# Kernel optimization log

Hardware: AMD Instinct MI355X
Metric: run time of the kernel (lower is better)

## Reference

```python
import jax, jax.numpy as jnp
import numpy as np

IMG, P, CIN, D, K, L, H, FF, B = 512, 32, 3, 256, 8192, 6, 8, 1024, 32
GRID = IMG // P  # 16
DH = D // H
EPS = 1e-5


def _ln(x, w, b):
    m = x.mean(-1, keepdims=True)
    v = ((x - m) ** 2).mean(-1, keepdims=True)
    return (x - m) / jnp.sqrt(v + EPS) * w + b


def _mha(x, wqkv, bqkv, wo, bo):
    # x: (S, Bt, D) -- axis 0 is the attention axis (torch batch_first=False quirk)
    S, Bt, _ = x.shape
    qkv = x @ wqkv.T + bqkv
    q, k, v = jnp.split(qkv, 3, axis=-1)
    q = q.reshape(S, Bt, H, DH)
    k = k.reshape(S, Bt, H, DH)
    v = v.reshape(S, Bt, H, DH)
    scores = jnp.einsum('sbhd,tbhd->bhst', q, k) / jnp.sqrt(jnp.float32(DH))
    attn = jax.nn.softmax(scores, axis=-1)
    o = jnp.einsum('bhst,tbhd->sbhd', attn, v).reshape(S, Bt, D)
    return o @ wo.T + bo


def _conv_t(x, w, b, stride=2, pad=1):
    # w uses torch ConvTranspose2d layout (Cin, Cout, kH, kW)
    kH = w.shape[2]
    wf = jnp.flip(w, (2, 3)).transpose(1, 0, 2, 3)  # -> (Cout, Cin, kH, kW)
    y = jax.lax.conv_general_dilated(
        x, wf, window_strides=(1, 1),
        padding=[(kH - 1 - pad, kH - 1 - pad)] * 2,
        lhs_dilation=(stride, stride),
        dimension_numbers=('NCHW', 'OIHW', 'NCHW'))
    return y + b[None, :, None, None]


def _forward(x, patch_w, patch_b, qkv_w, qkv_b, out_w, out_b, ln1_w, ln1_b,
             ln2_w, ln2_b, ff1_w, ff1_b, ff2_w, ff2_b, lnf_w, lnf_b, codebook,
             dec_w0, dec_b0, dec_w1, dec_b1, dec_w2, dec_b2, dec_w3, dec_b3):
    # patch embedding: conv stride=patch -> (B, D, G, G) -> (B, N, D)
    h = jax.lax.conv_general_dilated(
        x, patch_w, (P, P), 'VALID',
        dimension_numbers=('NCHW', 'OIHW', 'NCHW')) + patch_b[None, :, None, None]
    h = h.reshape(h.shape[0], D, -1).transpose(0, 2, 1)  # (B, N, D)
    # torch TransformerEncoderLayer default batch_first=False: attention runs
    # over axis 0 (image batch); faithfully replicated here. Post-norm, eval
    # mode (dropout=identity), exact gelu.
    for i in range(L):
        a = _mha(h, qkv_w[i], qkv_b[i], out_w[i], out_b[i])
        h = _ln(h + a, ln1_w[i], ln1_b[i])
        f = jax.nn.gelu(h @ ff1_w[i].T + ff1_b[i], approximate=False) @ ff2_w[i].T + ff2_b[i]
        h = _ln(h + f, ln2_w[i], ln2_b[i])
    h = _ln(h, lnf_w, lnf_b)
    # vector quantization: squared-distance argmin over codebook
    flat = h.reshape(-1, D)  # (B*N, D)
    d = ((flat ** 2).sum(-1, keepdims=True)
         - 2.0 * flat @ codebook.T
         + (codebook ** 2).sum(-1))  # (B*N, K)
    idx = jnp.argmin(d, axis=1)
    q = codebook[idx].reshape(h.shape)
    e_loss = jnp.mean((jax.lax.stop_gradient(q) - h) ** 2)
    q_loss = jnp.mean((q - jax.lax.stop_gradient(h)) ** 2)
    vq_loss = q_loss + 0.25 * e_loss
    q = h + jax.lax.stop_gradient(q - h)  # straight-through
    q = q.transpose(0, 2, 1).reshape(x.shape[0], D, GRID, GRID)
    y = jax.nn.relu(_conv_t(q, dec_w0, dec_b0))
    y = jax.nn.relu(_conv_t(y, dec_w1, dec_b1))
    y = jax.nn.relu(_conv_t(y, dec_w2, dec_b2))
    x_hat = jax.nn.sigmoid(_conv_t(y, dec_w3, dec_b3))
    return x_hat, vq_loss


def setup_inputs() -> dict:
    key = jax.random.key(0)
    ks = iter(jax.random.split(key, 64))
    nrm = lambda shape, s=0.02: jax.random.normal(next(ks), shape, jnp.float32) * s
    f32 = jnp.float32
    return {
        'x': jax.random.normal(next(ks), (B, CIN, IMG, IMG), f32),
        'patch_w': nrm((D, CIN, P, P)),
        'patch_b': jnp.zeros((D,), f32),
        'qkv_w': nrm((L, 3 * D, D)),
        'qkv_b': jnp.zeros((L, 3 * D), f32),
        'out_w': nrm((L, D, D)),
        'out_b': jnp.zeros((L, D), f32),
        'ln1_w': jnp.ones((L, D), f32),
        'ln1_b': jnp.zeros((L, D), f32),
        'ln2_w': jnp.ones((L, D), f32),
        'ln2_b': jnp.zeros((L, D), f32),
        'ff1_w': nrm((L, FF, D)),
        'ff1_b': jnp.zeros((L, FF), f32),
        'ff2_w': nrm((L, D, FF)),
        'ff2_b': jnp.zeros((L, D), f32),
        'lnf_w': jnp.ones((D,), f32),
        'lnf_b': jnp.zeros((D,), f32),
        'codebook': jax.random.uniform(next(ks), (K, D), f32, -1.0 / K, 1.0 / K),
        'dec_w0': nrm((D, 256, 4, 4)),
        'dec_b0': jnp.zeros((256,), f32),
        'dec_w1': nrm((256, 128, 4, 4)),
        'dec_b1': jnp.zeros((128,), f32),
        'dec_w2': nrm((128, 64, 4, 4)),
        'dec_b2': jnp.zeros((64,), f32),
        'dec_w3': nrm((64, CIN, 4, 4)),
        'dec_b3': jnp.zeros((CIN,), f32),
    }


def reference(x, patch_w, patch_b, qkv_w, qkv_b, out_w, out_b, ln1_w, ln1_b,
              ln2_w, ln2_b, ff1_w, ff1_b, ff2_w, ff2_b, lnf_w, lnf_b, codebook,
              dec_w0, dec_b0, dec_w1, dec_b1, dec_w2, dec_b2, dec_w3, dec_b3):
    return _forward(x, patch_w, patch_b, qkv_w, qkv_b, out_w, out_b, ln1_w,
                    ln1_b, ln2_w, ln2_b, ff1_w, ff1_b, ff2_w, ff2_b, lnf_w,
                    lnf_b, codebook, dec_w0, dec_b0, dec_w1, dec_b1, dec_w2,
                    dec_b2, dec_w3, dec_b3)
```

## Files before the change

kernel.cpp:

```cpp
#include <hip/hip_runtime.h>
#include <hip/hip_bf16.h>
#include <math.h>

typedef __hip_bfloat16 bf16;
typedef unsigned int u32;
typedef unsigned long long u64;
using short8 = __attribute__((ext_vector_type(8))) short;
using f32x4  = __attribute__((ext_vector_type(4))) float;

__device__ __forceinline__ float b2f(bf16 v){ return __bfloat162float(v); }
__device__ __forceinline__ bf16  f2b(float v){ return __float2bfloat16(v); }
__device__ __forceinline__ float plo(u32 u){ return __uint_as_float(u << 16); }
__device__ __forceinline__ float phi(u32 u){ return __uint_as_float(u & 0xffff0000u); }

__device__ __forceinline__ void gld16(const void* g, void* l)
{
  __builtin_amdgcn_global_load_lds(
      (const __attribute__((address_space(1))) u32*)g,
      (__attribute__((address_space(3))) u32*)l, 16, 0, 0);
}

__global__ void k_detect(const u32* probe, int* flag)
{
  if (threadIdx.x == 0 && blockIdx.x == 0)
    *flag = (*probe == 0x3F800000u) ? 0 : 1;
}

struct PPack { const void* s[25]; u32 off[26]; };
__global__ __launch_bounds__(256) void k_convall(PPack pp, bf16* P, const int* flag)
{
  const u32 i = blockIdx.x * 256 + threadIdx.x;
  if (i >= pp.off[25]) return;
  int lo = 0, hi = 25;
  while (hi - lo > 1) { const int mid = (lo + hi) >> 1; if (i >= pp.off[mid]) lo = mid; else hi = mid; }
  const u32 j = i - pp.off[lo];
  P[i] = *flag ? ((const bf16*)pp.s[lo])[j] : f2b(((const float*)pp.s[lo])[j]);
}

__global__ __launch_bounds__(256) void k_zero(u32* p, int n)
{
  const int i = blockIdx.x * 256 + threadIdx.x;
  if (i < n) p[i] = 0;
}

__global__ __launch_bounds__(128) void k_im2col(const void* x, bf16* A, const int* flag)
{
  const int m = blockIdx.y;
  const int k8 = blockIdx.x * 128 + threadIdx.x;
  const int k = k8 * 8;
  const int b = m >> 8, n = m & 255;
  const int gy = n >> 4, gx = n & 15;
  const int c = k >> 10, r = (k >> 5) & 31, pp = k & 31;
  const size_t src = (((size_t)(b * 3 + c) * 512) + gy * 32 + r) * 512 + gx * 32 + pp;
  bf16 ov[8];
  if (*flag) {
    const bf16* xp = (const bf16*)x + src;
    #pragma unroll
    for (int i = 0; i < 8; ++i) ov[i] = xp[i];
  } else {
    const float4 v0 = *reinterpret_cast<const float4*>((const float*)x + src);
    const float4 v1 = *reinterpret_cast<const float4*>((const float*)x + src + 4);
    ov[0]=f2b(v0.x); ov[1]=f2b(v0.y); ov[2]=f2b(v0.z); ov[3]=f2b(v0.w);
    ov[4]=f2b(v1.x); ov[5]=f2b(v1.y); ov[6]=f2b(v1.z); ov[7]=f2b(v1.w);
  }
  *reinterpret_cast<uint4*>(A + (size_t)m * 3072 + k) = *reinterpret_cast<const uint4*>(ov);
}

template<int EPI, int FM>
__global__ __launch_bounds__(256, 2) void gemm_t(
    const bf16* __restrict__ A, const bf16* __restrict__ Bw,
    const bf16* __restrict__ bias, const bf16* res, bf16* C,
    const float* __restrict__ cnorm, u64* __restrict__ ku,
    int M, int N, int K)
{
  constexpr int BM = FM * 32;
  __shared__ alignas(16) bf16 As[2][BM * 64];
  __shared__ alignas(16) bf16 Bs[2][128 * 64];
  const int tid = threadIdx.x;
  const int bn = blockIdx.x * 128, bm = blockIdx.y * BM;
  const int l = tid & 63, w = tid >> 6;
  const int wm = w >> 1, wn = w & 1;
  const int lg = l >> 4, lr = l & 15;
  const int sr8 = l >> 3;
  const int sch = (l & 7) ^ sr8;
  f32x4 acc[FM][4];
  #pragma unroll
  for (int fm = 0; fm < FM; ++fm)
    #pragma unroll
    for (int fn = 0; fn < 4; ++fn) acc[fm][fn] = (f32x4){0.f, 0.f, 0.f, 0.f};

  auto stage = [&](int bb, int k0) {
    char* ab = (char*)As[bb];
    char* bp = (char*)Bs[bb];
    #pragma unroll
    for (int it = 0; it < FM; ++it) {
      const int r = w * 8 + it * 32 + sr8;
      gld16(A + (size_t)(bm + r) * K + k0 + sch * 8, ab + w * 1024 + it * 4096);
    }
    #pragma unroll
    for (int it = 0; it < 4; ++it) {
      const int r = w * 8 + it * 32 + sr8;
      gld16(Bw + (size_t)(bn + r) * K + k0 + sch * 8, bp + w * 1024 + it * 4096);
    }
  };

  const int nt = K >> 6;
  stage(0, 0);
  __syncthreads();
  for (int t = 0; t < nt; ++t) {
    const int cur = t & 1;
    if (t + 1 < nt) stage(cur ^ 1, (t + 1) << 6);
    const char* ab = (const char*)As[cur];
    const char* bb = (const char*)Bs[cur];
    #pragma unroll
    for (int ks = 0; ks < 2; ++ks) {
      short8 af[FM], bfr[4];
      #pragma unroll
      for (int fm = 0; fm < FM; ++fm) {
        const int r = wm * (FM * 16) + fm * 16 + lr;
        af[fm] = *reinterpret_cast<const short8*>(ab + r * 128 + (((lg + ks * 4) ^ (r & 7)) * 16));
      }
      #pragma unroll
      for (int fn = 0; fn < 4; ++fn) {
        const int r = wn * 64 + fn * 16 + lr;
        bfr[fn] = *reinterpret_cast<const short8*>(bb + r * 128 + (((lg + ks * 4) ^ (r & 7)) * 16));
      }
      #pragma unroll
      for (int fm = 0; fm < FM; ++fm)
        #pragma unroll
        for (int fn = 0; fn < 4; ++fn)
          acc[fm][fn] = __builtin_amdgcn_mfma_f32_16x16x32_bf16(af[fm], bfr[fn], acc[fm][fn], 0, 0, 0);
    }
    __syncthreads();
  }

  if (EPI == 3) {
    __shared__ u64 skey[128][2];
    float cn4[4];
    #pragma unroll
    for (int fn = 0; fn < 4; ++fn) cn4[fn] = cnorm[bn + wn * 64 + fn * 16 + lr];
    #pragma unroll
    for (int fm = 0; fm < FM; ++fm) {
      #pragma unroll
      for (int r = 0; r < 4; ++r) {
        u64 best = ~0ull;
        #pragma unroll
        for (int fn = 0; fn < 4; ++fn) {
          const int col = bn + wn * 64 + fn * 16 + lr;
          const float d = cn4[fn] - 2.0f * acc[fm][fn][r];
          u32 u = __float_as_uint(d);
          u = (u & 0x80000000u) ? ~u : (u | 0x80000000u);
          const u64 key = ((u64)u << 32) | (u32)col;
          best = key < best ? key : best;
        }
        #pragma unroll
        for (int mk = 1; mk < 16; mk <<= 1) {
          const u64 o = __shfl_xor(best, mk, 64);
          best = o < best ? o : best;
        }
        if (lr == 0) skey[wm * 64 + fm * 16 + lg * 4 + r][wn] = best;
      }
    }
    __syncthreads();
    if (tid < 128) {
      const u64 a = skey[tid][0], b = skey[tid][1];
      ku[(size_t)blockIdx.x * M + bm + tid] = a < b ? a : b;
    }
  } else {
    #pragma unroll
    for (int fm = 0; fm < FM; ++fm) {
      const int m0 = bm + wm * (FM * 16) + fm * 16 + lg * 4;
      #pragma unroll
      for (int fn = 0; fn < 4; ++fn) {
        const int n = bn + wn * 64 + fn * 16 + lr;
        const float bs = b2f(bias[n]);
        #pragma unroll
        for (int r = 0; r < 4; ++r) {
          float v = acc[fm][fn][r] + bs;
          if (EPI == 1) v = 0.5f * v * (1.0f + erff(v * 0.70710678118654752f));
          if (EPI == 2) v += b2f(res[(size_t)(m0 + r) * N + n]);
          C[(size_t)(m0 + r) * N + n] = f2b(v);
        }
      }
    }
  }
}

__global__ __launch_bounds__(256) void k_vqmerge(
    const u64* __restrict__ ku, int* __restrict__ idx, int M, int NB)
{
  const int r = blockIdx.x * 256 + threadIdx.x;
  if (r >= M) return;
  u64 best = ku[r];
  for (int nb = 1; nb < NB; ++nb) {
    const u64 k = ku[(size_t)nb * M + r];
    best = k < best ? k : best;
  }
  idx[r] = (int)(best & 0xFFFFFFFFull);
}

__global__ __launch_bounds__(256) void k_cnorm(const bf16* __restrict__ cb, float* __restrict__ cn)
{
  const int j = blockIdx.x * 256 + threadIdx.x;
  const u32* p = (const u32*)(cb + (size_t)j * 256);
  float s = 0.f;
  for (int k = 0; k < 128; ++k) {
    const u32 v = p[k];
    const float a = plo(v), b = phi(v);
    s += a * a + b * b;
  }
  cn[j] = s;
}

__global__ __launch_bounds__(256) void k_ln(
    bf16* h, const bf16* w, const bf16* b)
{
  __shared__ float red[256];
  __shared__ float stat[2];
  const int row = blockIdx.x, d = threadIdx.x;
  const size_t base = (size_t)row * 256;
  const float x = b2f(h[base + d]);
  red[d] = x;
  __syncthreads();
  for (int off = 128; off > 0; off >>= 1) {
    if (d < off) red[d] += red[d + off];
    __syncthreads();
  }
  if (d == 0) stat[0] = red[0] * (1.0f / 256.0f);
  __syncthreads();
  const float m = stat[0];
  red[d] = (x - m) * (x - m);
  __syncthreads();
  for (int off = 128; off > 0; off >>= 1) {
    if (d < off) red[d] += red[d + off];
    __syncthreads();
  }
  if (d == 0) stat[1] = 1.0f / sqrtf(red[0] * (1.0f / 256.0f) + 1e-5f);
  __syncthreads();
  h[base + d] = f2b((x - m) * stat[1] * b2f(w[d]) + b2f(b[d]));
}

__global__ __launch_bounds__(256) void k_attn(
    const bf16* qkv, bf16* o)
{
  __shared__ float qs[32][33], ks[32][33], vs[32][33], ps[32][33];
  __shared__ float rs[32];
  const int bt = blockIdx.x, hd = blockIdx.y;
  const int tid = threadIdx.x;
  for (int e = 0; e < 4; ++e) {
    const int elem = tid + 256 * e;
    const int s = elem >> 5, c = elem & 31;
    const bf16* p = qkv + (size_t)(s * 256 + bt) * 768 + hd * 32 + c;
    qs[s][c] = b2f(p[0]);
    ks[s][c] = b2f(p[256]);
    vs[s][c] = b2f(p[512]);
  }
  __syncthreads();
  const int s = tid >> 3, j = tid & 7;
  float sc[4];
  #pragma unroll
  for (int e = 0; e < 4; ++e) {
    const int t = j + 8 * e;
    float v = 0.f;
    #pragma unroll
    for (int dd = 0; dd < 32; ++dd) v += qs[s][dd] * ks[t][dd];
    sc[e] = v * 0.17677669529663687f;
  }
  float mx = fmaxf(fmaxf(sc[0], sc[1]), fmaxf(sc[2], sc[3]));
  #pragma unroll
  for (int mk = 1; mk < 8; mk <<= 1) mx = fmaxf(mx, __shfl_xor(mx, mk, 64));
  float sm = 0.f; float ex[4];
  #pragma unroll
  for (int e = 0; e < 4; ++e) { ex[e] = expf(sc[e] - mx); sm += ex[e]; }
  #pragma unroll
  for (int mk = 1; mk < 8; mk <<= 1) sm += __shfl_xor(sm, mk, 64);
  #pragma unroll
  for (int e = 0; e < 4; ++e) ps[s][j + 8 * e] = ex[e];
  if (j == 0) rs[s] = 1.0f / sm;
  __syncthreads();
  #pragma unroll
  for (int e = 0; e < 4; ++e) {
    const int dd = j + 8 * e;
    float acc = 0.f;
    #pragma unroll
    for (int t = 0; t < 32; ++t) acc += ps[s][t] * vs[t][dd];
    o[(size_t)(s * 256 + bt) * 256 + hd * 32 + dd] = f2b(acc * rs[s]);
  }
}

__global__ __launch_bounds__(256) void k_gather(
    const bf16* h, const bf16* cb, const int* idx, bf16* a0, float* lsum)
{
  __shared__ float red[256];
  const int row = blockIdx.x, d = threadIdx.x;
  const int code = idx[row] & 8191;
  const float q = b2f(cb[(size_t)code * 256 + d]);
  const float x = b2f(h[(size_t)row * 256 + d]);
  red[d] = (q - x) * (q - x);
  __syncthreads();
  for (int off = 128; off > 0; off >>= 1) {
    if (d < off) red[d] += red[d + off];
    __syncthreads();
  }
  if (d == 0) lsum[row] = red[0];
  const int b = row >> 8, n = row & 255;
  const int y = n >> 4, xc = n & 15;
  a0[(((size_t)b * 18 + y + 1) * 18 + (xc + 1)) * 256 + d] = f2b(q);
}

__global__ __launch_bounds__(256) void k_loss(const float* lsum, float* out)
{
  __shared__ float red[256];
  const int tid = threadIdx.x;
  float v = 0.f;
  for (int i = 0; i < 32; ++i) v += lsum[tid + 256 * i];
  red[tid] = v;
  __syncthreads();
  for (int off = 128; off > 0; off >>= 1) {
    if (tid < off) red[tid] += red[tid + off];
    __syncthreads();
  }
  if (tid == 0)
    out[0] = red[0] * (1.25f / 2097152.0f);
}

__global__ __launch_bounds__(256) void k_wtrans(
    const bf16* __restrict__ w, bf16* __restrict__ wt,
    int Cin, int lCin, int CoutR, int CoutP)
{
  const int K = Cin << 2;
  const int total = 4 * CoutP * K;
  const int i = blockIdx.x * 256 + threadIdx.x;
  if (i >= total) return;
  const int p = i / (CoutP * K);
  const int rem = i - p * (CoutP * K);
  const int co = rem / K;
  const int k = rem - co * K;
  const int tap = k >> lCin, ci = k - (tap << lCin);
  const int py = p >> 1, px = p & 1, ty = tap >> 1, tx = tap & 1;
  bf16 v = f2b(0.f);
  if (co < CoutR)
    v = w[(((size_t)ci * CoutR + co) * 4 + py + 2 * ty) * 4 + px + 2 * tx];
  wt[i] = v;
}

__global__ __launch_bounds__(256, 2) void convt64(
    const bf16* __restrict__ in, const bf16* __restrict__ Wt,
    const bf16* __restrict__ bias, bf16* __restrict__ outp,
    int H, int lH, int Cin, int lCin, int Cout)
{
  __shared__ alignas(16) bf16 As[2][128 * 64];
  __shared__ alignas(16) bf16 Bs[2][64 * 64];
  const int tid = threadIdx.x;
  const int pz = blockIdx.z;
  const int py = pz >> 1, px = pz & 1;
  const int K = Cin << 2;
  const int bn = blockIdx.x * 64, bm = blockIdx.y * 128;
  const bf16* Bw = Wt + (size_t)pz * Cout * K;
  const int l = tid & 63, w = tid >> 6;
  const int wm = w >> 1, wn = w & 1;
  const int lg = l >> 4, lr = l & 15;
  const int sr8 = l >> 3;
  const int sch = (l & 7) ^ sr8;
  const int Hp = H + 2;
  f32x4 acc[4][2];
  #pragma unroll
  for (int fm = 0; fm < 4; ++fm)
    #pragma unroll
    for (int fn = 0; fn < 2; ++fn) acc[fm][fn] = (f32x4){0.f, 0.f, 0.f, 0.f};

  size_t pixbase[4];
  #pragma unroll
  for (int it = 0; it < 4; ++it) {
    const int m = bm + w * 8 + it * 32 + sr8;
    const int b = m >> (2 * lH);
    const int rem = m & ((1 << (2 * lH)) - 1);
    const int jj = rem >> lH, ii = rem & (H - 1);
    pixbase[it] = ((size_t)(b * Hp + jj) * Hp + ii);
  }

  auto stage = [&](int bb, int k0) {
    char* ab = (char*)As[bb];
    char* bp = (char*)Bs[bb];
    const int tap = k0 >> lCin;
    const int ty = tap >> 1, tx = tap & 1;
    const int sy = (1 - py) + (1 - ty);
    const int sx = (1 - px) + (1 - tx);
    const int ci0 = (k0 - (tap << lCin)) + sch * 8;
    #pragma unroll
    for (int it = 0; it < 4; ++it)
      gld16(in + (pixbase[it] + (size_t)sy * Hp + sx) * Cin + ci0,
            ab + w * 1024 + it * 4096);
    #pragma unroll
    for (int it = 0; it < 2; ++it) {
      const int r = w * 8 + it * 32 + sr8;
      gld16(Bw + (size_t)(bn + r) * K + k0 + sch * 8, bp + w * 1024 + it * 4096);
    }
  };

  const int nt = K >> 6;
  stage(0, 0);
  __syncthreads();
  for (int t = 0; t < nt; ++t) {
    const int cur = t & 1;
    if (t + 1 < nt) stage(cur ^ 1, (t + 1) << 6);
    const char* ab = (const char*)As[cur];
    const char* bb = (const char*)Bs[cur];
    #pragma unroll
    for (int ks = 0; ks < 2; ++ks) {
      short8 af[4], bfr[2];
      #pragma unroll
      for (int fm = 0; fm < 4; ++fm) {
        const int r = wm * 64 + fm * 16 + lr;
        af[fm] = *reinterpret_cast<const short8*>(ab + r * 128 + (((lg + ks * 4) ^ (r & 7)) * 16));
      }
      #pragma unroll
      for (int fn = 0; fn < 2; ++fn) {
        const int r = wn * 32 + fn * 16 + lr;
        bfr[fn] = *reinterpret_cast<const short8*>(bb + r * 128 + (((lg + ks * 4) ^ (r & 7)) * 16));
      }
      #pragma unroll
      for (int fm = 0; fm < 4; ++fm)
        #pragma unroll
        for (int fn = 0; fn < 2; ++fn)
          acc[fm][fn] = __builtin_amdgcn_mfma_f32_16x16x32_bf16(af[fm], bfr[fn], acc[fm][fn], 0, 0, 0);
    }
    __syncthreads();
  }

  const int Ho = 2 * H, Hop = Ho + 2;
  #pragma unroll
  for (int fm = 0; fm < 4; ++fm) {
    const int m0 = bm + wm * 64 + fm * 16 + lg * 4;
    #pragma unroll
    for (int fn = 0; fn < 2; ++fn) {
      const int n = bn + wn * 32 + fn * 16 + lr;
      #pragma unroll
      for (int r = 0; r < 4; ++r) {
        const int m = m0 + r;
        const int b = m >> (2 * lH);
        const int rem = m & ((1 << (2 * lH)) - 1);
        const int jj = rem >> lH, ii = rem & (H - 1);
        const int oy = 2 * jj + (1 - py), ox = 2 * ii + (1 - px);
        const float v = fmaxf(acc[fm][fn][r] + b2f(bias[n]), 0.f);
        outp[((size_t)(b * Hop + oy + 1) * Hop + ox + 1) * Cout + n] = f2b(v);
      }
    }
  }
}

__global__ __launch_bounds__(256) void k_dec3(
    const bf16* __restrict__ a3, const bf16* __restrict__ wt3,
    const bf16* __restrict__ bias, float* __restrict__ xhat, int chunkBase)
{
  __shared__ float wl[4][3][256];
  const int tid = threadIdx.x;
  for (int i = tid; i < 3072; i += 256) {
    const int pz = i / 768;
    const int rem = i - pz * 768;
    const int co = rem >> 8, k = rem & 255;
    wl[pz][co][k] = b2f(wt3[(pz * 3 + co) * 256 + k]);
  }
  __syncthreads();
  const int b = blockIdx.y;
  const int t = blockIdx.x;
  const int oy = (t >> 4) * 16 + (tid >> 4);
  const int ox = (t & 15) * 16 + (tid & 15);
  const int py = (oy + 1) & 1, px = (ox + 1) & 1;
  const int jj = (oy - 1 + py) >> 1, ii = (ox - 1 + px) >> 1;
  const int pz = py * 2 + px;
  float a0 = 0.f, a1 = 0.f, a2 = 0.f;
  #pragma unroll
  for (int ty = 0; ty < 2; ++ty) {
    #pragma unroll
    for (int tx = 0; tx < 2; ++tx) {
      const int sy = (1 - py) + (1 - ty), sx = (1 - px) + (1 - tx);
      const int tap = ty * 2 + tx;
      const u32* ip = (const u32*)(a3 + ((size_t)(b * 130 + jj + sy) * 130 + ii + sx) * 64);
      const float* w0 = &wl[pz][0][tap * 64];
      const float* w1 = &wl[pz][1][tap * 64];
      const float* w2 = &wl[pz][2][tap * 64];
      #pragma unroll
      for (int kk = 0; kk < 32; ++kk) {
        const u32 v = ip[kk];
        const float e0 = plo(v), e1 = phi(v);
        a0 += e0 * w0[2 * kk] + e1 * w0[2 * kk + 1];
        a1 += e0 * w1[2 * kk] + e1 * w1[2 * kk + 1];
        a2 += e0 * w2[2 * kk] + e1 * w2[2 * kk + 1];
      }
    }
  }
  const int n = chunkBase + b;
  const size_t ob = (size_t)n * 3 * 65536 + oy * 256 + ox;
  xhat[ob]           = 1.0f / (1.0f + expf(-(a0 + b2f(bias[0]))));
  xhat[ob + 65536]   = 1.0f / (1.0f + expf(-(a1 + b2f(bias[1]))));
  xhat[ob + 131072]  = 1.0f / (1.0f + expf(-(a2 + b2f(bias[2]))));
}

extern "C" void kernel_launch(void* const* d_in, const int* in_sizes, int n_in,
                              void* d_out, int out_size, void* d_ws, size_t ws_size,
                              hipStream_t stream)
{
  float* xhat = (float*)d_out;
  float* lossout = xhat + (out_size - 1);

  const size_t NEED = 130195456;
  if (ws_size < NEED) return;

  char* ws = (char*)d_ws;
  int*   flag  = (int*)  (ws + 0);
  float* lsum  = (float*)(ws + 1024);
  int*   idx   = (int*)  (ws + 65536);
  u64*   ku    = (u64*)  (ws + 131072);
  bf16*  P     = (bf16*) (ws + 8519680);
  bf16*  WT    = (bf16*) (ws + 27262976);
  float* cnorm = (float*)(ws + 30900224);
  bf16*  hbuf  = (bf16*) (ws + 31457280);
  bf16*  A_im  = (bf16*) (ws + 35651584);
  bf16*  qkvb  = (bf16*) (ws + 35651584);
  bf16*  obuf  = (bf16*) (ws + 48234496);
  bf16*  ffb   = (bf16*) (ws + 52428800);
  bf16*  a0    = (bf16*) (ws + 35651584);
  bf16*  a1    = (bf16*) (ws + 40960000);
  bf16*  a2    = (bf16*) (ws + 59899904);
  bf16*  a3    = (bf16*) (ws + 95584256);

  k_detect<<<1, 64, 0, stream>>>((const u32*)d_in[7], flag);

  size_t poff[26]; poff[1] = 0;
  for (int i = 2; i <= 25; ++i) poff[i] = poff[i - 1] + (size_t)in_sizes[i - 1];
  const size_t ptotal = poff[25] + (size_t)in_sizes[25];
  PPack pp;
  for (int i = 0; i < 25; ++i) { pp.s[i] = d_in[i + 1]; pp.off[i] = (u32)poff[i + 1]; }
  pp.off[25] = (u32)ptotal;
  k_convall<<<(int)((ptotal + 255) / 256), 256, 0, stream>>>(pp, P, flag);

  const bf16 *patch_w = P + poff[1],  *patch_b = P + poff[2];
  const bf16 *qkv_w   = P + poff[3],  *qkv_b   = P + poff[4];
  const bf16 *out_w   = P + poff[5],  *out_b   = P + poff[6];
  const bf16 *ln1_w   = P + poff[7],  *ln1_b   = P + poff[8];
  const bf16 *ln2_w   = P + poff[9],  *ln2_b   = P + poff[10];
  const bf16 *ff1_w   = P + poff[11], *ff1_b   = P + poff[12];
  const bf16 *ff2_w   = P + poff[13], *ff2_b   = P + poff[14];
  const bf16 *lnf_w   = P + poff[15], *lnf_b   = P + poff[16];
  const bf16 *codebook= P + poff[17];
  const bf16 *dec_w0  = P + poff[18], *dec_b0  = P + poff[19];
  const bf16 *dec_w1  = P + poff[20], *dec_b1  = P + poff[21];
  const bf16 *dec_w2  = P + poff[22], *dec_b2  = P + poff[23];
  const bf16 *dec_w3  = P + poff[24], *dec_b3  = P + poff[25];

  bf16* wt0 = WT;
  bf16* wt1 = wt0 + 1048576;
  bf16* wt2 = wt1 + 524288;
  bf16* wt3 = wt2 + 131072;
  k_wtrans<<<(1048576 + 255) / 256, 256, 0, stream>>>(dec_w0, wt0, 256, 8, 256, 256);
  k_wtrans<<<(524288 + 255) / 256, 256, 0, stream>>>(dec_w1, wt1, 256, 8, 128, 128);
  k_wtrans<<<(131072 + 255) / 256, 256, 0, stream>>>(dec_w2, wt2, 128, 7, 64, 64);
  k_wtrans<<<(3072 + 255) / 256, 256, 0, stream>>>(dec_w3, wt3, 64, 6, 3, 3);
  k_cnorm<<<32, 256, 0, stream>>>(codebook, cnorm);

  k_im2col<<<dim3(3, 8192), 128, 0, stream>>>(d_in[0], A_im, flag);
  gemm_t<0, 1><<<dim3(2, 256), 256, 0, stream>>>(
      A_im, patch_w, patch_b, nullptr, hbuf, nullptr, nullptr, 8192, 256, 3072);

  for (int l = 0; l < 6; ++l) {
    gemm_t<0, 2><<<dim3(6, 128), 256, 0, stream>>>(
        hbuf, qkv_w + (size_t)l * 768 * 256, qkv_b + l * 768, nullptr, qkvb,
        nullptr, nullptr, 8192, 768, 256);
    k_attn<<<dim3(256, 8), 256, 0, stream>>>(qkvb, obuf);
    gemm_t<2, 1><<<dim3(2, 256), 256, 0, stream>>>(
        obuf, out_w + (size_t)l * 256 * 256, out_b + l * 256, hbuf, hbuf,
        nullptr, nullptr, 8192, 256, 256);
    k_ln<<<8192, 256, 0, stream>>>(hbuf, ln1_w + l * 256, ln1_b + l * 256);
    gemm_t<1, 2><<<dim3(8, 128), 256, 0, stream>>>(
        hbuf, ff1_w + (size_t)l * 1024 * 256, ff1_b + l * 1024, nullptr, ffb,
        nullptr, nullptr, 8192, 1024, 256);
    gemm_t<2, 1><<<dim3(2, 256), 256, 0, stream>>>(
        ffb, ff2_w + (size_t)l * 256 * 1024, ff2_b + l * 256, hbuf, hbuf,
        nullptr, nullptr, 8192, 256, 1024);
    k_ln<<<8192, 256, 0, stream>>>(hbuf, ln2_w + l * 256, ln2_b + l * 256);
  }
  k_ln<<<8192, 256, 0, stream>>>(hbuf, lnf_w, lnf_b);

  gemm_t<3, 4><<<dim3(64, 64), 256, 0, stream>>>(
      hbuf, codebook, nullptr, nullptr, nullptr, cnorm, ku, 8192, 8192, 256);
  k_vqmerge<<<32, 256, 0, stream>>>(ku, idx, 8192, 64);

  k_zero<<<(1327104 + 255) / 256, 256, 0, stream>>>((u32*)a0, 1327104);
  k_gather<<<8192, 256, 0, stream>>>(hbuf, codebook, idx, a0, lsum);
  k_loss<<<1, 256, 0, stream>>>(lsum, lossout);

  k_zero<<<(4734976 + 255) / 256, 256, 0, stream>>>((u32*)a1, 4734976);
  k_zero<<<(8921088 + 255) / 256, 256, 0, stream>>>((u32*)a2, 8921088);
  k_zero<<<(8652800 + 255) / 256, 256, 0, stream>>>((u32*)a3, 8652800);

  convt64<<<dim3(4, 64, 4), 256, 0, stream>>>(a0, wt0, dec_b0, a1, 16, 4, 256, 8, 256);
  convt64<<<dim3(2, 256, 4), 256, 0, stream>>>(a1, wt1, dec_b1, a2, 32, 5, 256, 8, 128);
  for (int c = 0; c < 2; ++c) {
    const bf16* a2c = a2 + (size_t)c * 16 * 66 * 66 * 128;
    convt64<<<dim3(1, 512, 4), 256, 0, stream>>>(a2c, wt2, dec_b2, a3, 64, 6, 128, 7, 64);
    k_dec3<<<dim3(256, 16), 256, 0, stream>>>(a3, wt3, dec_b3, xhat, c * 16);
  }
}
```

Before: 1.156 ms.

## Split-K narrow GEMMs into fp32 partials and fuse reduction with bias, residual, LayerNorm

The N=256 GEMMs (patch embed, attention out-proj, FF2) now use split-K over blockIdx.z and write fp32 partials. A new row kernel sums the partials, adds bias and residual, and applies LayerNorm in the same pass. This replaces the separate residual epilogue and k_ln launches and adds more blocks for the long-K GEMMs. The GEMM also gains a single-buffered mode for the short-K cases, which halves LDS so more blocks can be resident, at the cost of losing load/compute overlap. The trade-off is extra fp32 partial traffic to and from global memory in exchange for more parallelism and fewer bf16 round trips.

```diff
diff --git a/kernel.cpp b/kernel.cpp
--- a/kernel.cpp
+++ b/kernel.cpp
@@ -66,18 +66,20 @@
   *reinterpret_cast<uint4*>(A + (size_t)m * 3072 + k) = *reinterpret_cast<const uint4*>(ov);
 }
 
-template<int EPI, int FM>
+template<int EPI, int FM, bool DB>
 __global__ __launch_bounds__(256, 2) void gemm_t(
     const bf16* __restrict__ A, const bf16* __restrict__ Bw,
-    const bf16* __restrict__ bias, const bf16* res, bf16* C,
+    const bf16* __restrict__ bias, bf16* C, float* __restrict__ Cf,
     const float* __restrict__ cnorm, u64* __restrict__ ku,
-    int M, int N, int K)
+    int M, int N, int K, int Kc)
 {
   constexpr int BM = FM * 32;
-  __shared__ alignas(16) bf16 As[2][BM * 64];
-  __shared__ alignas(16) bf16 Bs[2][128 * 64];
+  __shared__ alignas(16) bf16 As[DB ? 2 : 1][BM * 64];
+  __shared__ alignas(16) bf16 Bs[DB ? 2 : 1][128 * 64];
   const int tid = threadIdx.x;
   const int bn = blockIdx.x * 128, bm = blockIdx.y * BM;
+  const int z = blockIdx.z;
+  const int kb = z * Kc;
   const int l = tid & 63, w = tid >> 6;
   const int wm = w >> 1, wn = w & 1;
   const int lg = l >> 4, lr = l & 15;
@@ -103,15 +105,9 @@
       gld16(Bw + (size_t)(bn + r) * K + k0 + sch * 8, bp + w * 1024 + it * 4096);
     }
   };
-
-  const int nt = K >> 6;
-  stage(0, 0);
-  __syncthreads();
-  for (int t = 0; t < nt; ++t) {
-    const int cur = t & 1;
-    if (t + 1 < nt) stage(cur ^ 1, (t + 1) << 6);
-    const char* ab = (const char*)As[cur];
-    const char* bb = (const char*)Bs[cur];
+  auto compute = [&](int bb) {
+    const char* ab = (const char*)As[bb];
+    const char* bp = (const char*)Bs[bb];
     #pragma unroll
     for (int ks = 0; ks < 2; ++ks) {
       short8 af[FM], bfr[4];
@@ -123,7 +119,7 @@
       #pragma unroll
       for (int fn = 0; fn < 4; ++fn) {
         const int r = wn * 64 + fn * 16 + lr;
-        bfr[fn] = *reinterpret_cast<const short8*>(bb + r * 128 + (((lg + ks * 4) ^ (r & 7)) * 16));
+        bfr[fn] = *reinterpret_cast<const short8*>(bp + r * 128 + (((lg + ks * 4) ^ (r & 7)) * 16));
       }
       #pragma unroll
       for (int fm = 0; fm < FM; ++fm)
@@ -131,7 +127,25 @@
         for (int fn = 0; fn < 4; ++fn)
           acc[fm][fn] = __builtin_amdgcn_mfma_f32_16x16x32_bf16(af[fm], bfr[fn], acc[fm][fn], 0, 0, 0);
     }
-    __syncthreads();
+  };
+
+  const int nt = Kc >> 6;
+  if (DB) {
+    stage(0, kb);
+    __syncthreads();
+    for (int t = 0; t < nt; ++t) {
+      const int cur = t & 1;
+      if (t + 1 < nt) stage(cur ^ 1, kb + ((t + 1) << 6));
+      compute(cur);
+      __syncthreads();
+    }
+  } else {
+    for (int t = 0; t < nt; ++t) {
+      if (t) __syncthreads();
+      stage(0, kb + (t << 6));
+      __syncthreads();
+      compute(0);
+    }
   }
 
   if (EPI == 3) {
@@ -166,6 +180,18 @@
       const u64 a = skey[tid][0], b = skey[tid][1];
       ku[(size_t)blockIdx.x * M + bm + tid] = a < b ? a : b;
     }
+  } else if (EPI == 4) {
+    #pragma unroll
+    for (int fm = 0; fm < FM; ++fm) {
+      const int m0 = bm + wm * (FM * 16) + fm * 16 + lg * 4;
+      #pragma unroll
+      for (int fn = 0; fn < 4; ++fn) {
+        const int n = bn + wn * 64 + fn * 16 + lr;
+        #pragma unroll
+        for (int r = 0; r < 4; ++r)
+          Cf[((size_t)z * M + m0 + r) * N + n] = acc[fm][fn][r];
+      }
+    }
   } else {
     #pragma unroll
     for (int fm = 0; fm < FM; ++fm) {
@@ -178,12 +204,45 @@
         for (int r = 0; r < 4; ++r) {
           float v = acc[fm][fn][r] + bs;
           if (EPI == 1) v = 0.5f * v * (1.0f + erff(v * 0.70710678118654752f));
-          if (EPI == 2) v += b2f(res[(size_t)(m0 + r) * N + n]);
           C[(size_t)(m0 + r) * N + n] = f2b(v);
         }
       }
     }
   }
+}
+
+template<bool DOLN>
+__global__ __launch_bounds__(256) void k_lnred(
+    const float* __restrict__ Pf, const bf16* __restrict__ bias,
+    const bf16* res, const bf16* __restrict__ lw, const bf16* __restrict__ lb,
+    bf16* h, int kc)
+{
+  __shared__ float red[256];
+  __shared__ float stat[2];
+  const int row = blockIdx.x, d = threadIdx.x;
+  float s = 0.f;
+  for (int z = 0; z < kc; ++z) s += Pf[((size_t)z * 8192 + row) * 256 + d];
+  s += b2f(bias[d]);
+  if (res) s += b2f(res[(size_t)row * 256 + d]);
+  if (!DOLN) { h[(size_t)row * 256 + d] = f2b(s); return; }
+  red[d] = s;
+  __syncthreads();
+  for (int off = 128; off > 0; off >>= 1) {
+    if (d < off) red[d] += red[d + off];
+    __syncthreads();
+  }
+  if (d == 0) stat[0] = red[0] * (1.0f / 256.0f);
+  __syncthreads();
+  const float m = stat[0];
+  red[d] = (s - m) * (s - m);
+  __syncthreads();
+  for (int off = 128; off > 0; off >>= 1) {
+    if (d < off) red[d] += red[d + off];
+    __syncthreads();
+  }
+  if (d == 0) stat[1] = 1.0f / sqrtf(red[0] * (1.0f / 256.0f) + 1e-5f);
+  __syncthreads();
+  h[(size_t)row * 256 + d] = f2b((s - m) * stat[1] * b2f(lw[d]) + b2f(lb[d]));
 }
 
 __global__ __launch_bounds__(256) void k_vqmerge(
@@ -520,6 +579,7 @@
   bf16*  qkvb  = (bf16*) (ws + 35651584);
   bf16*  obuf  = (bf16*) (ws + 48234496);
   bf16*  ffb   = (bf16*) (ws + 52428800);
+  float* Pf    = (float*)(ws + 85983232);
   bf16*  a0    = (bf16*) (ws + 35651584);
   bf16*  a1    = (bf16*) (ws + 40960000);
   bf16*  a2    = (bf16*) (ws + 59899904);
@@ -560,30 +620,34 @@
   k_cnorm<<<32, 256, 0, stream>>>(codebook, cnorm);
 
   k_im2col<<<dim3(3, 8192), 128, 0, stream>>>(d_in[0], A_im, flag);
-  gemm_t<0, 1><<<dim3(2, 256), 256, 0, stream>>>(
-      A_im, patch_w, patch_b, nullptr, hbuf, nullptr, nullptr, 8192, 256, 3072);
+  gemm_t<4, 2, true><<<dim3(2, 128, 4), 256, 0, stream>>>(
+      A_im, patch_w, nullptr, nullptr, Pf, nullptr, nullptr, 8192, 256, 3072, 768);
+  k_lnred<false><<<8192, 256, 0, stream>>>(
+      Pf, patch_b, nullptr, nullptr, nullptr, hbuf, 4);
 
   for (int l = 0; l < 6; ++l) {
-    gemm_t<0, 2><<<dim3(6, 128), 256, 0, stream>>>(
-        hbuf, qkv_w + (size_t)l * 768 * 256, qkv_b + l * 768, nullptr, qkvb,
-        nullptr, nullptr, 8192, 768, 256);
+    gemm_t<0, 2, false><<<dim3(6, 128, 1), 256, 0, stream>>>(
+        hbuf, qkv_w + (size_t)l * 768 * 256, qkv_b + l * 768, qkvb, nullptr,
+        nullptr, nullptr, 8192, 768, 256, 256);
     k_attn<<<dim3(256, 8), 256, 0, stream>>>(qkvb, obuf);
-    gemm_t<2, 1><<<dim3(2, 256), 256, 0, stream>>>(
-        obuf, out_w + (size_t)l * 256 * 256, out_b + l * 256, hbuf, hbuf,
-        nullptr, nullptr, 8192, 256, 256);
-    k_ln<<<8192, 256, 0, stream>>>(hbuf, ln1_w + l * 256, ln1_b + l * 256);
-    gemm_t<1, 2><<<dim3(8, 128), 256, 0, stream>>>(
-        hbuf, ff1_w + (size_t)l * 1024 * 256, ff1_b + l * 1024, nullptr, ffb,
-        nullptr, nullptr, 8192, 1024, 256);
-    gemm_t<2, 1><<<dim3(2, 256), 256, 0, stream>>>(
-        ffb, ff2_w + (size_t)l * 256 * 1024, ff2_b + l * 256, hbuf, hbuf,
-        nullptr, nullptr, 8192, 256, 1024);
-    k_ln<<<8192, 256, 0, stream>>>(hbuf, ln2_w + l * 256, ln2_b + l * 256);
+    gemm_t<4, 2, false><<<dim3(2, 128, 1), 256, 0, stream>>>(
+        obuf, out_w + (size_t)l * 256 * 256, nullptr, nullptr, Pf,
+        nullptr, nullptr, 8192, 256, 256, 256);
+    k_lnred<true><<<8192, 256, 0, stream>>>(
+        Pf, out_b + l * 256, hbuf, ln1_w + l * 256, ln1_b + l * 256, hbuf, 1);
+    gemm_t<1, 2, false><<<dim3(8, 128, 1), 256, 0, stream>>>(
+        hbuf, ff1_w + (size_t)l * 1024 * 256, ff1_b + l * 1024, ffb, nullptr,
+        nullptr, nullptr, 8192, 1024, 256, 256);
+    gemm_t<4, 2, false><<<dim3(2, 128, 4), 256, 0, stream>>>(
+        ffb, ff2_w + (size_t)l * 256 * 1024, nullptr, nullptr, Pf,
+        nullptr, nullptr, 8192, 256, 1024, 256);
+    k_lnred<true><<<8192, 256, 0, stream>>>(
+        Pf, ff2_b + l * 256, hbuf, ln2_w + l * 256, ln2_b + l * 256, hbuf, 4);
   }
   k_ln<<<8192, 256, 0, stream>>>(hbuf, lnf_w, lnf_b);
 
-  gemm_t<3, 4><<<dim3(64, 64), 256, 0, stream>>>(
-      hbuf, codebook, nullptr, nullptr, nullptr, cnorm, ku, 8192, 8192, 256);
+  gemm_t<3, 4, false><<<dim3(64, 64, 1), 256, 0, stream>>>(
+      hbuf, codebook, nullptr, nullptr, nullptr, cnorm, ku, 8192, 8192, 256, 256);
   k_vqmerge<<<32, 256, 0, stream>>>(ku, idx, 8192, 64);
 
   k_zero<<<(1327104 + 255) / 256, 256, 0, stream>>>((u32*)a0, 1327104);
```

Result: faster. 1.116 ms (-3.5%).
